# Kernel optimization log

Measured on AMD Instinct MI355X. Metric: run time of the kernel, lower is better.

## Reference

```python
import jax, jax.numpy as jnp
import numpy as np

B, S, D = 4, 1024, 1024
H, DK = 16, 64

def setup_inputs() -> dict:
    key = jax.random.key(0)
    ks = jax.random.split(key, 12)
    s = lambda k, shape, scale: (jax.random.normal(k, shape, dtype=jnp.float32) * scale)
    inp = {
        "query": s(ks[0], (B, S, D), 1.0),
        "key":   s(ks[1], (B, S, D), 1.0),
        "value": s(ks[2], (B, S, D), 1.0),
        # per-head query projections stacked: [H, D, DK]
        "Wq": s(ks[3], (H, D, DK), D ** -0.5),
        "bq": jnp.zeros((H, DK), jnp.float32),
        # shared key / value projections (MQA)
        "Wk": s(ks[4], (D, DK), D ** -0.5),
        "bk": jnp.zeros((DK,), jnp.float32),
        "Wv": s(ks[5], (D, DK), D ** -0.5),
        "bv": jnp.zeros((DK,), jnp.float32),
        # combine_heads: Dense(key_dim) applied to concat of H head outputs
        "Wc": s(ks[6], (H * DK, DK), (H * DK) ** -0.5),
        "bc": jnp.zeros((DK,), jnp.float32),
    }
    return inp


def reference(query, key, value, Wq, bq, Wk, bk, Wv, bv, Wc, bc):
    # per-head query projections, batched over heads: [B,H,S,DK]
    q = jnp.einsum('bsd,hdk->bhsk', query, Wq) + bq[None, :, None, :]
    # shared K/V (multi-query attention): [B,S,DK]
    k = jnp.einsum('bsd,dk->bsk', key, Wk) + bk
    v = jnp.einsum('bsd,dk->bsk', value, Wv) + bv
    scale = 1.0 / jnp.sqrt(jnp.asarray(DK, q.dtype))
    # scores: [B,H,S,S], K broadcast across heads
    scores = jnp.einsum('bhsk,btk->bhst', q, k) * scale
    attn = jax.nn.softmax(scores, axis=-1)
    # head outputs: [B,H,S,DK]
    out_h = jnp.einsum('bhst,btk->bhsk', attn, v)
    # concat heads along last axis (head order preserved): [B,S,H*DK]
    concat = out_h.transpose(0, 2, 1, 3).reshape(B, S, H * DK)
    output = concat @ Wc + bc  # [B,S,DK]; dropout=0.0 -> identity
    return output, attn
```

## Files before the change

kernel.cpp:

```cpp
#include <hip/hip_runtime.h>

typedef __bf16 bf16;
typedef __attribute__((ext_vector_type(4))) float f32x4;
typedef __attribute__((ext_vector_type(8))) bf16 bf16x8;
typedef __attribute__((ext_vector_type(4))) bf16 bf16x4;

constexpr int Bc = 4, Sc = 1024, Dc = 1024, Hc = 16, DKc = 64;


__device__ __forceinline__ void stage64(bf16* s, const void* g, int ld, int f32src) {
  const int t = threadIdx.x;
#pragma unroll
  for (int i = 0; i < 2; ++i) {
    const int G = t + i * 256;
    const int r = G >> 3, gr = G & 7;
    bf16x8 o;
    if (f32src) {
      const float* gp = (const float*)g + (long)r * ld + gr * 8;
      const f32x4 a = *(const f32x4*)gp;
      const f32x4 b = *(const f32x4*)(gp + 4);
      o[0]=(bf16)a[0]; o[1]=(bf16)a[1]; o[2]=(bf16)a[2]; o[3]=(bf16)a[3];
      o[4]=(bf16)b[0]; o[5]=(bf16)b[1]; o[6]=(bf16)b[2]; o[7]=(bf16)b[3];
    } else {
      o = *(const bf16x8*)((const bf16*)g + (long)r * ld + gr * 8);
    }
    *(bf16x8*)(s + r * 64 + ((gr * 8) ^ ((r & 7) << 3))) = o;
  }
}

__device__ __forceinline__ bf16x8 frag_ld(const bf16* s, int row, int kofs) {
  const int lane = threadIdx.x & 63;
  const int c0 = kofs + (((lane >> 4) & 3) << 2);
  const int sw = (row & 7) << 3;
  union { bf16x8 v8; bf16x4 v4[2]; } u;
  u.v4[0] = *(const bf16x4*)(s + row * 64 + (c0 ^ sw));
  u.v4[1] = *(const bf16x4*)(s + row * 64 + ((c0 + 16) ^ sw));
  return u.v8;
}


__global__ __launch_bounds__(256) void transpose_weights(
    const float* __restrict__ Wq, const float* __restrict__ Wk,
    const float* __restrict__ Wv, const float* __restrict__ Wc,
    bf16* __restrict__ WqT, bf16* __restrict__ WkT,
    bf16* __restrict__ WvT, bf16* __restrict__ WcT) {
  const int i = blockIdx.x * 256 + threadIdx.x;
  if (i < 1048576) {
    const int h = i >> 16, r = i & 65535, dk = r >> 10, d = r & 1023;
    WqT[i] = (bf16)Wq[(h << 16) + d * 64 + dk];
  } else if (i < 1114112) {
    const int j = i - 1048576, dk = j >> 10, d = j & 1023;
    WkT[j] = (bf16)Wk[d * 64 + dk];
  } else if (i < 1179648) {
    const int j = i - 1114112, dk = j >> 10, d = j & 1023;
    WvT[j] = (bf16)Wv[d * 64 + dk];
  } else if (i < 1245184) {
    const int j = i - 1179648, dk = j >> 10, c = j & 1023;
    WcT[j] = (bf16)Wc[c * 64 + dk];
  }
}

__global__ __launch_bounds__(256) void proj_kernel(
    const float* __restrict__ query, const float* __restrict__ key,
    const float* __restrict__ value, const bf16* __restrict__ WqT,
    const bf16* __restrict__ WkT, const bf16* __restrict__ WvT,
    const float* __restrict__ bq, const float* __restrict__ bk,
    const float* __restrict__ bv, bf16* __restrict__ q_cat,
    bf16* __restrict__ k_proj, bf16* __restrict__ vTp) {
  const int bid = blockIdx.x;
  const void* A; const void* BT; bf16* C; const float* bias;
  int m0, n0, ldA, ldBT, ldC, aF32, bF32, biasM;
  if (bid < 1024) {
    m0 = (bid >> 4) << 6; n0 = (bid & 15) << 6;
    A = query; ldA = 1024; aF32 = 1;
    BT = WqT;  ldBT = 1024; bF32 = 0;
    C = q_cat; ldC = 1024; bias = bq; biasM = 0;
  } else if (bid < 1088) {
    m0 = (bid - 1024) << 6; n0 = 0;
    A = key;    ldA = 1024; aF32 = 1;
    BT = WkT;   ldBT = 1024; bF32 = 0;
    C = k_proj; ldC = 64; bias = bk; biasM = 0;
  } else {
    const int j = bid - 1088;
    m0 = 0; n0 = (j & 15) << 6;
    A = WvT; ldA = 1024; aF32 = 0;
    BT = value + ((long)(j >> 4) << 20); ldBT = 1024; bF32 = 1;
    C = vTp + ((long)(j >> 4) << 16); ldC = 1024; bias = bv; biasM = 1;
  }

  __shared__ bf16 sA[2][4096];
  __shared__ bf16 sB[2][4096];
  const int lane = threadIdx.x & 63;
  const int w = threadIdx.x >> 6;

  f32x4 acc[4];
#pragma unroll
  for (int nb = 0; nb < 4; ++nb) acc[nb] = (f32x4){0.f, 0.f, 0.f, 0.f};

  stage64(sA[0], aF32 ? (const void*)((const float*)A + (long)m0 * ldA)
                      : (const void*)((const bf16*)A + (long)m0 * ldA), ldA, aF32);
  stage64(sB[0], bF32 ? (const void*)((const float*)BT + (long)n0 * ldBT)
                      : (const void*)((const bf16*)BT + (long)n0 * ldBT), ldBT, bF32);
  __syncthreads();

  for (int it = 0; it < 16; ++it) {
    const int p = it & 1;
    if (it < 15) {
      const int kk = (it + 1) * 64;
      stage64(sA[p ^ 1], aF32 ? (const void*)((const float*)A + (long)m0 * ldA + kk)
                              : (const void*)((const bf16*)A + (long)m0 * ldA + kk), ldA, aF32);
      stage64(sB[p ^ 1], bF32 ? (const void*)((const float*)BT + (long)n0 * ldBT + kk)
                              : (const void*)((const bf16*)BT + (long)n0 * ldBT + kk), ldBT, bF32);
    }
#pragma unroll
    for (int ks = 0; ks < 2; ++ks) {
      const bf16x8 af = frag_ld(sA[p], 16 * w + (lane & 15), ks * 32);
#pragma unroll
      for (int nb = 0; nb < 4; ++nb) {
        const bf16x8 bfr = frag_ld(sB[p], nb * 16 + (lane & 15), ks * 32);
        acc[nb] = __builtin_amdgcn_mfma_f32_16x16x32_bf16(af, bfr, acc[nb], 0, 0, 0);
      }
    }
    __syncthreads();
  }

  const int rbase = m0 + 16 * w + ((lane >> 4) << 2);
#pragma unroll
  for (int nb = 0; nb < 4; ++nb) {
    const int col = n0 + nb * 16 + (lane & 15);
    const float bn = biasM ? 0.f : bias[col];
#pragma unroll
    for (int r = 0; r < 4; ++r) {
      const int row = rbase + r;
      C[(long)row * ldC + col] = (bf16)(acc[nb][r] + (biasM ? bias[row] : bn));
    }
  }
}

__global__ __launch_bounds__(256) void combine_kernel(
    const bf16* __restrict__ concat, const bf16* __restrict__ WcT,
    const float* __restrict__ bc, float* __restrict__ out0) {
  const int m0 = blockIdx.x * 64;
  __shared__ bf16 sA[2][4096];
  __shared__ bf16 sB[2][4096];
  const int lane = threadIdx.x & 63;
  const int w = threadIdx.x >> 6;

  f32x4 acc[4];
#pragma unroll
  for (int nb = 0; nb < 4; ++nb) acc[nb] = (f32x4){0.f, 0.f, 0.f, 0.f};

  stage64(sA[0], concat + (long)m0 * 1024, 1024, 0);
  stage64(sB[0], WcT, 1024, 0);
  __syncthreads();
  for (int it = 0; it < 16; ++it) {
    const int p = it & 1;
    if (it < 15) {
      const int kk = (it + 1) * 64;
      stage64(sA[p ^ 1], concat + (long)m0 * 1024 + kk, 1024, 0);
      stage64(sB[p ^ 1], WcT + kk, 1024, 0);
    }
#pragma unroll
    for (int ks = 0; ks < 2; ++ks) {
      const bf16x8 af = frag_ld(sA[p], 16 * w + (lane & 15), ks * 32);
#pragma unroll
      for (int nb = 0; nb < 4; ++nb) {
        const bf16x8 bfr = frag_ld(sB[p], nb * 16 + (lane & 15), ks * 32);
        acc[nb] = __builtin_amdgcn_mfma_f32_16x16x32_bf16(af, bfr, acc[nb], 0, 0, 0);
      }
    }
    __syncthreads();
  }
  const int rbase = m0 + 16 * w + ((lane >> 4) << 2);
#pragma unroll
  for (int nb = 0; nb < 4; ++nb) {
    const int col = nb * 16 + (lane & 15);
    const float bn = bc[col];
#pragma unroll
    for (int r = 0; r < 4; ++r)
      out0[(long)(rbase + r) * 64 + col] = acc[nb][r] + bn;
  }
}

__global__ __launch_bounds__(256, 4) void attn_kernel(
    const bf16* __restrict__ q_cat, const bf16* __restrict__ k_proj,
    const bf16* __restrict__ vT, float* __restrict__ attn_out,
    bf16* __restrict__ concat) {
  const int s0 = blockIdx.x * 64;
  const int h = blockIdx.y, b = blockIdx.z;
  const int lane = threadIdx.x & 63;
  const int w = threadIdx.x >> 6;
  const float scale = 0.125f;

  __shared__ bf16 sQ[4096];
  __shared__ bf16 sK[2][4096];
  __shared__ bf16 sV[2][4096];

  const bf16* qp = q_cat + (long)(b * Sc + s0) * 1024 + h * 64;
  const bf16* kp = k_proj + (long)b * Sc * DKc;
  const bf16* vp = vT + (long)b * DKc * Sc;
  float* ao = attn_out + ((long)(b * Hc + h) * Sc + s0) * Sc;
  bf16* co = concat + (long)(b * Sc + s0) * (Hc * DKc) + h * DKc;

  stage64(sQ, qp, 1024, 0);
  stage64(sK[0], kp, DKc, 0);
  __syncthreads();

  const int rowq = w * 16 + (lane & 15);
  bf16x8 qf[2];
  qf[0] = frag_ld(sQ, rowq, 0);
  qf[1] = frag_ld(sQ, rowq, 32);

  float lsum = 0.f;

  for (int tc = 0; tc < 16; ++tc) {
    const int p = tc & 1;
    if (tc < 15) stage64(sK[p ^ 1], kp + (long)(tc + 1) * 64 * DKc, DKc, 0);
    f32x4 sc[4];
#pragma unroll
    for (int nb = 0; nb < 4; ++nb) sc[nb] = (f32x4){0.f, 0.f, 0.f, 0.f};
#pragma unroll
    for (int ks = 0; ks < 2; ++ks)
#pragma unroll
      for (int nb = 0; nb < 4; ++nb) {
        const bf16x8 kf = frag_ld(sK[p], nb * 16 + (lane & 15), ks * 32);
        sc[nb] = __builtin_amdgcn_mfma_f32_16x16x32_bf16(kf, qf[ks], sc[nb], 0, 0, 0);
      }
#pragma unroll
    for (int nb = 0; nb < 4; ++nb)
#pragma unroll
      for (int r = 0; r < 4; ++r) lsum += __expf(sc[nb][r] * scale);
    __syncthreads();
  }

  lsum += __shfl_xor(lsum, 16, 64);
  lsum += __shfl_xor(lsum, 32, 64);
  const float invl = 1.f / lsum;

  f32x4 oacc[4];
#pragma unroll
  for (int nb = 0; nb < 4; ++nb) oacc[nb] = (f32x4){0.f, 0.f, 0.f, 0.f};

  stage64(sK[0], kp, DKc, 0);
  stage64(sV[0], vp, Sc, 0);
  __syncthreads();
  const int c0q = (lane >> 4) << 2;
  for (int tc = 0; tc < 16; ++tc) {
    const int p = tc & 1;
    if (tc < 15) {
      stage64(sK[p ^ 1], kp + (long)(tc + 1) * 64 * DKc, DKc, 0);
      stage64(sV[p ^ 1], vp + (tc + 1) * 64, Sc, 0);
    }
    f32x4 sc[4];
#pragma unroll
    for (int nb = 0; nb < 4; ++nb) sc[nb] = (f32x4){0.f, 0.f, 0.f, 0.f};
#pragma unroll
    for (int ks = 0; ks < 2; ++ks)
#pragma unroll
      for (int nb = 0; nb < 4; ++nb) {
        const bf16x8 kf = frag_ld(sK[p], nb * 16 + (lane & 15), ks * 32);
        sc[nb] = __builtin_amdgcn_mfma_f32_16x16x32_bf16(kf, qf[ks], sc[nb], 0, 0, 0);
      }
    float pe[4][4];
#pragma unroll
    for (int nb = 0; nb < 4; ++nb)
#pragma unroll
      for (int r = 0; r < 4; ++r) pe[nb][r] = __expf(sc[nb][r] * scale);
#pragma unroll
    for (int nb = 0; nb < 4; ++nb) {
      f32x4 av;
#pragma unroll
      for (int r = 0; r < 4; ++r) av[r] = pe[nb][r] * invl;
      *(f32x4*)(ao + (long)rowq * Sc + tc * 64 + nb * 16 + c0q) = av;
    }
    bf16x8 pa[2];
#pragma unroll
    for (int hi = 0; hi < 2; ++hi)
#pragma unroll
      for (int j = 0; j < 4; ++j) {
        pa[hi][j]     = (bf16)pe[2 * hi][j];
        pa[hi][4 + j] = (bf16)pe[2 * hi + 1][j];
      }
#pragma unroll
    for (int ks = 0; ks < 2; ++ks)
#pragma unroll
      for (int nb = 0; nb < 4; ++nb) {
        const bf16x8 vf = frag_ld(sV[p], nb * 16 + (lane & 15), ks * 32);
        oacc[nb] = __builtin_amdgcn_mfma_f32_16x16x32_bf16(pa[ks], vf, oacc[nb], 0, 0, 0);
      }
    __syncthreads();
  }

  float invo[4];
#pragma unroll
  for (int r = 0; r < 4; ++r)
    invo[r] = __shfl(invl, ((lane >> 4) << 2) + r, 64);
#pragma unroll
  for (int nb = 0; nb < 4; ++nb) {
#pragma unroll
    for (int r = 0; r < 4; ++r) {
      const int row = w * 16 + ((lane >> 4) << 2) + r;
      const int col = nb * 16 + (lane & 15);
      co[(long)row * (Hc * DKc) + col] = (bf16)(oacc[nb][r] * invo[r]);
    }
  }
}


extern "C" void kernel_launch(void* const* d_in, const int* in_sizes, int n_in,
                              void* d_out, int out_size, void* d_ws, size_t ws_size,
                              hipStream_t stream) {
  const float* query = (const float*)d_in[0];
  const float* key   = (const float*)d_in[1];
  const float* value = (const float*)d_in[2];
  const float* Wq = (const float*)d_in[3];
  const float* bq = (const float*)d_in[4];
  const float* Wk = (const float*)d_in[5];
  const float* bk = (const float*)d_in[6];
  const float* Wv = (const float*)d_in[7];
  const float* bv = (const float*)d_in[8];
  const float* Wc = (const float*)d_in[9];
  const float* bc = (const float*)d_in[10];

  bf16* WqT    = (bf16*)d_ws;
  bf16* WkT    = WqT + 1048576;
  bf16* WvT    = WkT + 65536;
  bf16* WcT    = WvT + 65536;
  bf16* q_cat  = WcT + 65536;
  bf16* k_proj = q_cat + 4194304;
  bf16* vTp    = k_proj + 262144;
  bf16* concat = vTp + 262144;

  float* out0 = (float*)d_out;
  float* attn = out0 + (long)Bc * Sc * DKc;

  transpose_weights<<<4864, 256, 0, stream>>>(Wq, Wk, Wv, Wc, WqT, WkT, WvT, WcT);

  proj_kernel<<<1152, 256, 0, stream>>>(query, key, value, WqT, WkT, WvT,
                                        bq, bk, bv, q_cat, k_proj, vTp);

  attn_kernel<<<dim3(16, 16, 4), 256, 0, stream>>>(q_cat, k_proj, vTp, attn, concat);

  combine_kernel<<<64, 256, 0, stream>>>(concat, WcT, bc, out0);
}
```

Baseline: 191.3 us.

## Cache exp scores in shared memory to skip second QK pass

The attention kernel now computes Q·K^T once, stores the unnormalized exp probabilities as bf16 in a 64KB shared buffer, and reuses them for both the attn output write and the P·V product, instead of recomputing scores in a second pass. Each block handles 32 query rows, with two wave pairs splitting the key tiles; row sums and partial outputs are reduced through shared memory. The 1/sqrt(dk) scale is folded into Wq and bq during the weight transpose. The cost is large LDS use, which lowers occupancy, extra barriers, and attn values now carry bf16 rounding of the probabilities.

```diff
diff --git a/kernel.cpp b/kernel.cpp
--- a/kernel.cpp
+++ b/kernel.cpp
@@ -47,7 +47,7 @@
   const int i = blockIdx.x * 256 + threadIdx.x;
   if (i < 1048576) {
     const int h = i >> 16, r = i & 65535, dk = r >> 10, d = r & 1023;
-    WqT[i] = (bf16)Wq[(h << 16) + d * 64 + dk];
+    WqT[i] = (bf16)(Wq[(h << 16) + d * 64 + dk] * 0.125f);
   } else if (i < 1114112) {
     const int j = i - 1048576, dk = j >> 10, d = j & 1023;
     WkT[j] = (bf16)Wk[d * 64 + dk];
@@ -70,22 +70,23 @@
   const int bid = blockIdx.x;
   const void* A; const void* BT; bf16* C; const float* bias;
   int m0, n0, ldA, ldBT, ldC, aF32, bF32, biasM;
+  float bscale;
   if (bid < 1024) {
     m0 = (bid >> 4) << 6; n0 = (bid & 15) << 6;
     A = query; ldA = 1024; aF32 = 1;
     BT = WqT;  ldBT = 1024; bF32 = 0;
-    C = q_cat; ldC = 1024; bias = bq; biasM = 0;
+    C = q_cat; ldC = 1024; bias = bq; biasM = 0; bscale = 0.125f;
   } else if (bid < 1088) {
     m0 = (bid - 1024) << 6; n0 = 0;
     A = key;    ldA = 1024; aF32 = 1;
     BT = WkT;   ldBT = 1024; bF32 = 0;
-    C = k_proj; ldC = 64; bias = bk; biasM = 0;
+    C = k_proj; ldC = 64; bias = bk; biasM = 0; bscale = 1.f;
   } else {
     const int j = bid - 1088;
     m0 = 0; n0 = (j & 15) << 6;
     A = WvT; ldA = 1024; aF32 = 0;
     BT = value + ((long)(j >> 4) << 20); ldBT = 1024; bF32 = 1;
-    C = vTp + ((long)(j >> 4) << 16); ldC = 1024; bias = bv; biasM = 1;
+    C = vTp + ((long)(j >> 4) << 16); ldC = 1024; bias = bv; biasM = 1; bscale = 1.f;
   }
 
   __shared__ bf16 sA[2][4096];
@@ -128,7 +129,7 @@
 #pragma unroll
   for (int nb = 0; nb < 4; ++nb) {
     const int col = n0 + nb * 16 + (lane & 15);
-    const float bn = biasM ? 0.f : bias[col];
+    const float bn = biasM ? 0.f : bias[col] * bscale;
 #pragma unroll
     for (int r = 0; r < 4; ++r) {
       const int row = rbase + r;
@@ -182,40 +183,53 @@
   }
 }
 
-__global__ __launch_bounds__(256, 4) void attn_kernel(
+__global__ __launch_bounds__(256) void attn_kernel(
     const bf16* __restrict__ q_cat, const bf16* __restrict__ k_proj,
     const bf16* __restrict__ vT, float* __restrict__ attn_out,
     bf16* __restrict__ concat) {
-  const int s0 = blockIdx.x * 64;
+  const int s0 = blockIdx.x * 32;
   const int h = blockIdx.y, b = blockIdx.z;
   const int lane = threadIdx.x & 63;
   const int w = threadIdx.x >> 6;
-  const float scale = 0.125f;
-
-  __shared__ bf16 sQ[4096];
-  __shared__ bf16 sK[2][4096];
-  __shared__ bf16 sV[2][4096];
-
-  const bf16* qp = q_cat + (long)(b * Sc + s0) * 1024 + h * 64;
+  const int g = w >> 1, j = w & 1;
+
+  __shared__ bf16 sP[16][2048];
+  __shared__ bf16 sKV[2][4096];
+
   const bf16* kp = k_proj + (long)b * Sc * DKc;
   const bf16* vp = vT + (long)b * DKc * Sc;
   float* ao = attn_out + ((long)(b * Hc + h) * Sc + s0) * Sc;
   bf16* co = concat + (long)(b * Sc + s0) * (Hc * DKc) + h * DKc;
 
-  stage64(sQ, qp, 1024, 0);
-  stage64(sK[0], kp, DKc, 0);
-  __syncthreads();
-
-  const int rowq = w * 16 + (lane & 15);
+  const int c0q = (lane >> 4) << 2;
+  const int sl = g * 16 + (lane & 15);
+  const int swz = (sl & 7) << 3;
+
+  const bf16* qrow = q_cat + (long)(b * Sc + s0 + sl) * 1024 + h * 64;
   bf16x8 qf[2];
-  qf[0] = frag_ld(sQ, rowq, 0);
-  qf[1] = frag_ld(sQ, rowq, 32);
+  {
+    union { bf16x8 v8; bf16x4 v4[2]; } u0, u1;
+    u0.v4[0] = *(const bf16x4*)(qrow + c0q);
+    u0.v4[1] = *(const bf16x4*)(qrow + c0q + 16);
+    u1.v4[0] = *(const bf16x4*)(qrow + c0q + 32);
+    u1.v4[1] = *(const bf16x4*)(qrow + c0q + 48);
+    qf[0] = u0.v8; qf[1] = u1.v8;
+  }
 
   float lsum = 0.f;
 
-  for (int tc = 0; tc < 16; ++tc) {
-    const int p = tc & 1;
-    if (tc < 15) stage64(sK[p ^ 1], kp + (long)(tc + 1) * 64 * DKc, DKc, 0);
+  for (int r = 0; r < 8; ++r) {
+    __syncthreads();
+#pragma unroll
+    for (int i = 0; i < 4; ++i) {
+      const int G = threadIdx.x + i * 256;
+      const int tile = G >> 9, gi = G & 511;
+      const int row = gi >> 3, c8 = (gi & 7) * 8;
+      const bf16x8 v = *(const bf16x8*)(kp + ((long)(2 * r + tile) << 12) + row * 64 + c8);
+      *(bf16x8*)(&sKV[tile][row * 64 + (c8 ^ ((row & 7) << 3))]) = v;
+    }
+    __syncthreads();
+    const int tc = 2 * r + j;
     f32x4 sc[4];
 #pragma unroll
     for (int nb = 0; nb < 4; ++nb) sc[nb] = (f32x4){0.f, 0.f, 0.f, 0.f};
@@ -223,86 +237,89 @@
     for (int ks = 0; ks < 2; ++ks)
 #pragma unroll
       for (int nb = 0; nb < 4; ++nb) {
-        const bf16x8 kf = frag_ld(sK[p], nb * 16 + (lane & 15), ks * 32);
+        const bf16x8 kf = frag_ld(sKV[j], nb * 16 + (lane & 15), ks * 32);
         sc[nb] = __builtin_amdgcn_mfma_f32_16x16x32_bf16(kf, qf[ks], sc[nb], 0, 0, 0);
       }
-#pragma unroll
-    for (int nb = 0; nb < 4; ++nb)
-#pragma unroll
-      for (int r = 0; r < 4; ++r) lsum += __expf(sc[nb][r] * scale);
-    __syncthreads();
-  }
-
+    bf16* tp = &sP[tc][0];
+#pragma unroll
+    for (int nb = 0; nb < 4; ++nb) {
+      bf16x4 pb;
+#pragma unroll
+      for (int r4 = 0; r4 < 4; ++r4) {
+        const float p = __expf(sc[nb][r4]);
+        lsum += p;
+        pb[r4] = (bf16)p;
+      }
+      *(bf16x4*)(tp + sl * 64 + ((nb * 16 + c0q) ^ swz)) = pb;
+    }
+  }
+
+  __syncthreads();
   lsum += __shfl_xor(lsum, 16, 64);
   lsum += __shfl_xor(lsum, 32, 64);
-  const float invl = 1.f / lsum;
+  float* red = (float*)&sKV[0][0];
+  if (lane < 16) red[j * 32 + g * 16 + lane] = lsum;
+  __syncthreads();
+  const float invl = 1.f / (red[g * 16 + (lane & 15)] + red[32 + g * 16 + (lane & 15)]);
 
   f32x4 oacc[4];
 #pragma unroll
   for (int nb = 0; nb < 4; ++nb) oacc[nb] = (f32x4){0.f, 0.f, 0.f, 0.f};
 
-  stage64(sK[0], kp, DKc, 0);
-  stage64(sV[0], vp, Sc, 0);
-  __syncthreads();
-  const int c0q = (lane >> 4) << 2;
-  for (int tc = 0; tc < 16; ++tc) {
-    const int p = tc & 1;
-    if (tc < 15) {
-      stage64(sK[p ^ 1], kp + (long)(tc + 1) * 64 * DKc, DKc, 0);
-      stage64(sV[p ^ 1], vp + (tc + 1) * 64, Sc, 0);
-    }
-    f32x4 sc[4];
-#pragma unroll
-    for (int nb = 0; nb < 4; ++nb) sc[nb] = (f32x4){0.f, 0.f, 0.f, 0.f};
+  for (int r = 0; r < 8; ++r) {
+    __syncthreads();
+#pragma unroll
+    for (int i = 0; i < 4; ++i) {
+      const int G = threadIdx.x + i * 256;
+      const int tile = G >> 9, gi = G & 511;
+      const int row = gi >> 3, c8 = (gi & 7) * 8;
+      const bf16x8 v = *(const bf16x8*)(vp + (long)row * 1024 + (2 * r + tile) * 64 + c8);
+      *(bf16x8*)(&sKV[tile][row * 64 + (c8 ^ ((row & 7) << 3))]) = v;
+    }
+    __syncthreads();
+    const int tc = 2 * r + j;
+    const bf16* tp = &sP[tc][0];
+#pragma unroll
+    for (int nb = 0; nb < 4; ++nb) {
+      const bf16x4 pb = *(const bf16x4*)(tp + sl * 64 + ((nb * 16 + c0q) ^ swz));
+      f32x4 av;
+#pragma unroll
+      for (int r4 = 0; r4 < 4; ++r4) av[r4] = (float)pb[r4] * invl;
+      *(f32x4*)(ao + (long)sl * Sc + tc * 64 + nb * 16 + c0q) = av;
+    }
+    bf16x8 pa[2];
+    pa[0] = frag_ld(tp, sl, 0);
+    pa[1] = frag_ld(tp, sl, 32);
 #pragma unroll
     for (int ks = 0; ks < 2; ++ks)
 #pragma unroll
       for (int nb = 0; nb < 4; ++nb) {
-        const bf16x8 kf = frag_ld(sK[p], nb * 16 + (lane & 15), ks * 32);
-        sc[nb] = __builtin_amdgcn_mfma_f32_16x16x32_bf16(kf, qf[ks], sc[nb], 0, 0, 0);
-      }
-    float pe[4][4];
+        const bf16x8 vf = frag_ld(sKV[j], nb * 16 + (lane & 15), ks * 32);
+        oacc[nb] = __builtin_amdgcn_mfma_f32_16x16x32_bf16(pa[ks], vf, oacc[nb], 0, 0, 0);
+      }
+  }
+
+  __syncthreads();
+  float* ored = (float*)&sKV[0][0];
+  if (j == 1) {
 #pragma unroll
     for (int nb = 0; nb < 4; ++nb)
 #pragma unroll
-      for (int r = 0; r < 4; ++r) pe[nb][r] = __expf(sc[nb][r] * scale);
-#pragma unroll
-    for (int nb = 0; nb < 4; ++nb) {
-      f32x4 av;
-#pragma unroll
-      for (int r = 0; r < 4; ++r) av[r] = pe[nb][r] * invl;
-      *(f32x4*)(ao + (long)rowq * Sc + tc * 64 + nb * 16 + c0q) = av;
-    }
-    bf16x8 pa[2];
-#pragma unroll
-    for (int hi = 0; hi < 2; ++hi)
-#pragma unroll
-      for (int j = 0; j < 4; ++j) {
-        pa[hi][j]     = (bf16)pe[2 * hi][j];
-        pa[hi][4 + j] = (bf16)pe[2 * hi + 1][j];
-      }
-#pragma unroll
-    for (int ks = 0; ks < 2; ++ks)
-#pragma unroll
-      for (int nb = 0; nb < 4; ++nb) {
-        const bf16x8 vf = frag_ld(sV[p], nb * 16 + (lane & 15), ks * 32);
-        oacc[nb] = __builtin_amdgcn_mfma_f32_16x16x32_bf16(pa[ks], vf, oacc[nb], 0, 0, 0);
-      }
-    __syncthreads();
-  }
-
-  float invo[4];
-#pragma unroll
-  for (int r = 0; r < 4; ++r)
-    invo[r] = __shfl(invl, ((lane >> 4) << 2) + r, 64);
-#pragma unroll
-  for (int nb = 0; nb < 4; ++nb) {
-#pragma unroll
-    for (int r = 0; r < 4; ++r) {
-      const int row = w * 16 + ((lane >> 4) << 2) + r;
-      const int col = nb * 16 + (lane & 15);
-      co[(long)row * (Hc * DKc) + col] = (bf16)(oacc[nb][r] * invo[r]);
-    }
+      for (int r4 = 0; r4 < 4; ++r4)
+        ored[g * 1024 + nb * 256 + r4 * 64 + lane] = oacc[nb][r4];
+  }
+  __syncthreads();
+  if (j == 0) {
+    float invo[4];
+#pragma unroll
+    for (int r4 = 0; r4 < 4; ++r4) invo[r4] = __shfl(invl, c0q + r4, 64);
+#pragma unroll
+    for (int nb = 0; nb < 4; ++nb)
+#pragma unroll
+      for (int r4 = 0; r4 < 4; ++r4) {
+        const float v = (oacc[nb][r4] + ored[g * 1024 + nb * 256 + r4 * 64 + lane]) * invo[r4];
+        co[(long)(g * 16 + c0q + r4) * 1024 + nb * 16 + (lane & 15)] = (bf16)v;
+      }
   }
 }
 
@@ -339,7 +356,7 @@
   proj_kernel<<<1152, 256, 0, stream>>>(query, key, value, WqT, WkT, WvT,
                                         bq, bk, bv, q_cat, k_proj, vTp);
 
-  attn_kernel<<<dim3(16, 16, 4), 256, 0, stream>>>(q_cat, k_proj, vTp, attn, concat);
+  attn_kernel<<<dim3(32, 16, 4), 256, 0, stream>>>(q_cat, k_proj, vTp, attn, concat);
 
   combine_kernel<<<64, 256, 0, stream>>>(concat, WcT, bc, out0);
 }
```

After: 213.5 us. +11.6%, slower.
